# Kernel tuning notes

Measured on AMD Instinct MI355X. Metric: run time of the kernel, lower is better.

The kernel has to match this reference:

```python
import jax, jax.numpy as jnp
import numpy as np

P = 16
BN_EPS = 1e-5


def _to_patches(x, c, d):
    # [b, c*P, d*P] -> [b, c*d, P, P]
    b = x.shape[0]
    x = x.reshape(b, c, P, d, P).transpose(0, 1, 3, 2, 4)
    return x.reshape(b, c * d, P, P)


def _dwconv_block(x, dwk, g, bb, m, v, pwk):
    # depthwise 3x3 stride-2 conv (groups=C, no bias) + BN(eval) + GELU + 1x1 pointwise
    C = x.shape[1]
    y = jax.lax.conv_general_dilated(
        x, dwk[:, None, :, :], window_strides=(2, 2), padding=((1, 1), (1, 1)),
        feature_group_count=C, dimension_numbers=('NCHW', 'OIHW', 'NCHW'))
    y = g[None, :, None, None] * (y - m[None, :, None, None]) / jnp.sqrt(v + BN_EPS)[None, :, None, None] + bb[None, :, None, None]
    y = jax.nn.gelu(y, approximate=False)  # torch nn.GELU default = erf
    return jnp.einsum('bchw,oc->bohw', y, pwk)


def _forward(query, key, value, dw_k, bn_g, bn_b, bn_m, bn_v, pw_k, position, c1_w, c1_b, lin_w, lin_b):
    b, units, d_model = query.shape
    c = units // P
    d = d_model // P
    hp = P // 2  # spatial after stride-2 conv
    dk = hp * hp  # d_k = 64

    q = _to_patches(query, c, d)
    k = _to_patches(key, c, d)
    v = _to_patches(value, c, d)

    q = _dwconv_block(q, dw_k[0], bn_g[0], bn_b[0], bn_m[0], bn_v[0], pw_k[0])
    k = _dwconv_block(k, dw_k[1], bn_g[1], bn_b[1], bn_m[1], bn_v[1], pw_k[1])
    v = _dwconv_block(v, dw_k[2], bn_g[2], bn_b[2], bn_m[2], bn_v[2], pw_k[2])

    # [b, c*d, hp, hp] -> [b, c, d, hp*hp]
    q = q.reshape(b, c, d, dk)
    k = k.reshape(b, c, d, dk)
    v = v.reshape(b, c, d, dk)

    scores = jnp.einsum('bcdk,bcek->bcde', q, k) / jnp.sqrt(jnp.asarray(dk, q.dtype))
    scores = scores + position[None]  # learned additive position bias [c,d,d]
    p_attn = jax.nn.softmax(scores, axis=-1)
    x = jnp.einsum('bcde,bcek->bcdk', p_attn, v)  # [b, c, d, dk]

    # 'b c d (p1 p2) -> b (c p1) (d p2)', p1 = P//2
    x = x.reshape(b, c, d, hp, hp).transpose(0, 1, 3, 2, 4).reshape(b, c * hp, d * hp)

    # Conv1d(units//2 -> units, kernel 1) then Linear(d_model//2 -> d_model)
    x = jnp.einsum('bcl,oc->bol', x, c1_w) + c1_b[None, :, None]
    x = jnp.einsum('bcl,ol->bco', x, lin_w) + lin_b[None, None, :]
    return x


def setup_inputs() -> dict:
    key = jax.random.key(0)
    ks = jax.random.split(key, 8)
    b, units, d_model = 64, 32, 4096
    C = (units // P) * (d_model // P)  # 512
    inp = {
        'query': jax.random.normal(ks[0], (b, units, d_model), jnp.float32),
        'key': jax.random.normal(ks[1], (b, units, d_model), jnp.float32),
        'value': jax.random.normal(ks[2], (b, units, d_model), jnp.float32),
        'dw_k': jax.random.normal(ks[3], (3, C, 3, 3), jnp.float32) * 0.1,
        'bn_g': jnp.ones((3, C), jnp.float32),
        'bn_b': jnp.zeros((3, C), jnp.float32),
        'bn_m': jnp.zeros((3, C), jnp.float32),
        'bn_v': jnp.ones((3, C), jnp.float32),
        'pw_k': jax.random.normal(ks[4], (3, C, C), jnp.float32) * 0.02,
        'position': jax.random.normal(ks[5], (units // P, d_model // P, d_model // P), jnp.float32),
        'c1_w': jax.random.normal(ks[6], (units, units // 2), jnp.float32) * 0.1,
        'c1_b': jnp.zeros((units,), jnp.float32),
        'lin_w': jax.random.normal(ks[7], (d_model, d_model // 2), jnp.float32) * 0.02,
        'lin_b': jnp.zeros((d_model,), jnp.float32),
    }
    return inp


def reference(query, key, value, dw_k, bn_g, bn_b, bn_m, bn_v, pw_k, position, c1_w, c1_b, lin_w, lin_b):
    return _forward(query, key, value, dw_k, bn_g, bn_b, bn_m, bn_v, pw_k, position, c1_w, c1_b, lin_w, lin_b)
```

## Files before the change

### kernel.cpp

```cpp
#include <hip/hip_runtime.h>


typedef short s16x8 __attribute__((ext_vector_type(8)));
typedef float f32x4 __attribute__((ext_vector_type(4)));
typedef const __attribute__((address_space(1))) void* gas_t;
typedef __attribute__((address_space(3))) void* las_t;

__device__ __forceinline__ unsigned short f2bf(float x) {
  unsigned u = __float_as_uint(x);
  unsigned r = u + 0x7fffu + ((u >> 16) & 1u);
  return (unsigned short)(r >> 16);
}
__device__ __forceinline__ float bf2f(unsigned short h) {
  return __uint_as_float((unsigned)h << 16);
}

__global__ __launch_bounds__(256) void stageA_kernel(
    const float* __restrict__ xq, const float* __restrict__ xk,
    const float* __restrict__ xv, const float* __restrict__ dwk,
    const float* __restrict__ bng, const float* __restrict__ bnb,
    const float* __restrict__ bnm, const float* __restrict__ bnv,
    unsigned short* __restrict__ tTp)
{
  const int i  = blockIdx.y;
  const float* x = (i == 0) ? xq : (i == 1) ? xk : xv;
  const float* dwk_i = dwk + (size_t)i * 4608;
  const int co = i * 512;
  unsigned short* out = tTp + (size_t)i * 4194304;

  const int dd = threadIdx.x;
  const int oh = blockIdx.x & 7;
  const int cc = (blockIdx.x >> 3) & 1;
  const int b  = blockIdx.x >> 4;
  const int ch = cc * 256 + dd;

  float r[3][16];
#pragma unroll
  for (int kh = 0; kh < 3; ++kh) {
    int ih = 2 * oh - 1 + kh;
    if (ih >= 0 && ih <= 15) {
      const float* p = x + (size_t)(b * 32 + cc * 16 + ih) * 4096 + dd * 16;
#pragma unroll
      for (int jq = 0; jq < 4; ++jq)
        *(float4*)&r[kh][jq * 4] = *(const float4*)(p + jq * 4);
    } else {
#pragma unroll
      for (int j = 0; j < 16; ++j) r[kh][j] = 0.f;
    }
  }
  float w9[9];
#pragma unroll
  for (int j = 0; j < 9; ++j) w9[j] = dwk_i[ch * 9 + j];
  const float scale = bng[co + ch] / sqrtf(bnv[co + ch] + 1e-5f);
  const float shift = bnb[co + ch] - bnm[co + ch] * scale;

#pragma unroll
  for (int ow = 0; ow < 8; ++ow) {
    float acc = 0.f;
#pragma unroll
    for (int kh = 0; kh < 3; ++kh)
#pragma unroll
      for (int kw = 0; kw < 3; ++kw) {
        int iw = 2 * ow - 1 + kw;
        if (iw >= 0 && iw <= 15) acc = fmaf(r[kh][iw], w9[kh * 3 + kw], acc);
      }
    float y = acc * scale + shift;
    y = 0.5f * y * (1.f + erff(y * 0.70710678118654752f));
    unsigned short hi = f2bf(y);
    unsigned short lo = f2bf(y - bf2f(hi));
    size_t rowb = (size_t)(b * 64 + oh * 8 + ow) * 1024;
    out[rowb + ch] = hi;
    out[rowb + 512 + ch] = lo;
  }
}

__global__ __launch_bounds__(256) void split_kernel(
    const float* __restrict__ src, unsigned short* __restrict__ dst,
    int kshift, int total4)
{
  int i = blockIdx.x * 256 + threadIdx.x;
  if (i >= total4) return;
  size_t i4 = (size_t)i * 4;
  int K = 1 << kshift;
  int r = (int)(i4 >> kshift);
  int c = (int)(i4 & (size_t)(K - 1));
  float4 xv = *(const float4*)(src + i4);
  unsigned short h0 = f2bf(xv.x), h1 = f2bf(xv.y), h2 = f2bf(xv.z), h3 = f2bf(xv.w);
  unsigned short l0 = f2bf(xv.x - bf2f(h0)), l1 = f2bf(xv.y - bf2f(h1));
  unsigned short l2 = f2bf(xv.z - bf2f(h2)), l3 = f2bf(xv.w - bf2f(h3));
  unsigned short* dr = dst + (size_t)r * (K * 2) + c;
  uint2 hp, lp;
  hp.x = (unsigned)h0 | ((unsigned)h1 << 16);
  hp.y = (unsigned)h2 | ((unsigned)h3 << 16);
  lp.x = (unsigned)l0 | ((unsigned)l1 << 16);
  lp.y = (unsigned)l2 | ((unsigned)l3 << 16);
  *(uint2*)dr = hp;
  *(uint2*)(dr + K) = lp;
}

__global__ __launch_bounds__(256) void split_rs_kernel(
    const float* __restrict__ src, unsigned short* __restrict__ dst,
    float* __restrict__ rs, int total4)
{
  int i = blockIdx.x * 256 + threadIdx.x;
  if (i >= total4) return;
  size_t i4 = (size_t)i * 4;
  int r = (int)(i4 >> 11);
  int c = (int)(i4 & 2047);
  float4 xv = *(const float4*)(src + i4);
  unsigned short h0 = f2bf(xv.x), h1 = f2bf(xv.y), h2 = f2bf(xv.z), h3 = f2bf(xv.w);
  unsigned short l0 = f2bf(xv.x - bf2f(h0)), l1 = f2bf(xv.y - bf2f(h1));
  unsigned short l2 = f2bf(xv.z - bf2f(h2)), l3 = f2bf(xv.w - bf2f(h3));
  unsigned short* dr = dst + (size_t)r * 4096 + c;
  uint2 hp, lp;
  hp.x = (unsigned)h0 | ((unsigned)h1 << 16);
  hp.y = (unsigned)h2 | ((unsigned)h3 << 16);
  lp.x = (unsigned)l0 | ((unsigned)l1 << 16);
  lp.y = (unsigned)l2 | ((unsigned)l3 << 16);
  *(uint2*)dr = hp;
  *(uint2*)(dr + 2048) = lp;
  float s = xv.x + xv.y + xv.z + xv.w;
#pragma unroll
  for (int off = 1; off < 64; off <<= 1) s += __shfl_xor(s, off, 64);
  if ((threadIdx.x & 63) == 0) atomicAdd(&rs[r], s);
}

__global__ __launch_bounds__(256) void gemm_split_kernel(
    const unsigned short* __restrict__ Aall, const unsigned short* __restrict__ Ball,
    unsigned short* __restrict__ Call, int M, int N, int K)
{
  __shared__ unsigned short sA[4096];
  __shared__ unsigned short sB[8192];
  const int t = threadIdx.x;
  const int z = blockIdx.z;
  const unsigned short* A = Aall + (size_t)z * 524288;
  const unsigned short* B = Ball + (size_t)z * 4194304;
  unsigned short* Cq = Call + (size_t)z * 4194304;
  const int m0 = blockIdx.y * 64, n0 = blockIdx.x * 128;
  const int Kp = 3 * K, twoK = 2 * K, Km = K - 1;
  const int lane = t & 63;
  const int wv = t >> 6;
  const int colbase = wv * 32;
  const int h = lane & 15, g = lane >> 4;

  f32x4 acc[4][2];
#pragma unroll
  for (int mf = 0; mf < 4; ++mf)
#pragma unroll
    for (int nf = 0; nf < 2; ++nf)
      acc[mf][nf] = (f32x4){0.f, 0.f, 0.f, 0.f};

  int srow[4], sblk[4];
#pragma unroll
  for (int it = 0; it < 4; ++it) {
    int s = it * 256 + t;
    srow[it] = s >> 3;
    sblk[it] = (s & 7) ^ (srow[it] & 7);
  }
  const int ldsw = (t & 192) << 4;

  for (int k0 = 0; k0 < Kp; k0 += 64) {
    __syncthreads();
#pragma unroll
    for (int it = 0; it < 2; ++it) {
      int kp = k0 + sblk[it] * 8;
      int ac = (kp < twoK) ? (kp & Km) : (kp - K);
      const unsigned short* ga = A + (size_t)(m0 + srow[it]) * twoK + ac;
      __builtin_amdgcn_global_load_lds((gas_t)(const void*)ga,
          (las_t)(void*)((char*)sA + (it * 4096 + ldsw)), 16, 0, 0);
    }
#pragma unroll
    for (int it = 0; it < 4; ++it) {
      int kp = k0 + sblk[it] * 8;
      int bc = (kp < twoK) ? kp : (kp - twoK);
      const unsigned short* gb = B + (size_t)(n0 + srow[it]) * twoK + bc;
      __builtin_amdgcn_global_load_lds((gas_t)(const void*)gb,
          (las_t)(void*)((char*)sB + (it * 4096 + ldsw)), 16, 0, 0);
    }
    __syncthreads();

#pragma unroll
    for (int kk = 0; kk < 2; ++kk) {
      s16x8 af[4], bfr[2];
#pragma unroll
      for (int mf = 0; mf < 4; ++mf) {
        int arow = mf * 16 + h;
        int aoff = arow * 128 + (((kk * 4 + g) ^ (h & 7)) << 4);
        af[mf] = *(const s16x8*)((const char*)sA + aoff);
      }
#pragma unroll
      for (int nf = 0; nf < 2; ++nf) {
        int brow = colbase + nf * 16 + h;
        int boff = brow * 128 + (((kk * 4 + g) ^ (h & 7)) << 4);
        bfr[nf] = *(const s16x8*)((const char*)sB + boff);
      }
#pragma unroll
      for (int mf = 0; mf < 4; ++mf)
#pragma unroll
        for (int nf = 0; nf < 2; ++nf)
          acc[mf][nf] = __builtin_amdgcn_mfma_f32_16x16x32_bf16(
              af[mf], bfr[nf], acc[mf][nf], 0, 0, 0);
    }
  }

  if (z < 2) {
#pragma unroll
    for (int mf = 0; mf < 4; ++mf) {
      int mbase = m0 + mf * 16 + g * 4;
#pragma unroll
      for (int nf = 0; nf < 2; ++nf) {
        int n = n0 + colbase + nf * 16 + h;
        int bb = n >> 6, d = n & 63;
#pragma unroll
        for (int qq = 0; qq < 4; ++qq) {
          int m = mbase + qq;
          int cc = m >> 8;
          size_t rowb = ((size_t)(bb * 2 + cc) * 256 + (m & 255)) * 128;
          float vvv = acc[mf][nf][qq];
          unsigned short hi = f2bf(vvv);
          unsigned short lo = f2bf(vvv - bf2f(hi));
          Cq[rowb + d] = hi;
          Cq[rowb + 64 + d] = lo;
        }
      }
    }
  } else {
#pragma unroll
    for (int mf = 0; mf < 4; ++mf) {
      int mbase = m0 + mf * 16 + g * 4;
      int cc = mbase >> 8;
      int mc = mbase & 255;
#pragma unroll
      for (int nf = 0; nf < 2; ++nf) {
        int n = n0 + colbase + nf * 16 + h;
        int bb = n >> 6, d = n & 63;
        size_t rowb = ((size_t)(bb * 2 + cc) * 64 + d) * 512;
        ushort4 hv, lv;
        float v0 = acc[mf][nf][0], v1 = acc[mf][nf][1];
        float v2 = acc[mf][nf][2], v3 = acc[mf][nf][3];
        hv.x = f2bf(v0); hv.y = f2bf(v1); hv.z = f2bf(v2); hv.w = f2bf(v3);
        lv.x = f2bf(v0 - bf2f(hv.x)); lv.y = f2bf(v1 - bf2f(hv.y));
        lv.z = f2bf(v2 - bf2f(hv.z)); lv.w = f2bf(v3 - bf2f(hv.w));
        *(ushort4*)&Cq[rowb + mc] = hv;
        *(ushort4*)&Cq[rowb + 256 + mc] = lv;
      }
    }
  }
}

__global__ __launch_bounds__(512, 2) void gemm_final_kernel(
    const unsigned short* __restrict__ A, const unsigned short* __restrict__ B,
    float* __restrict__ C)
{
  __shared__ unsigned short lds[73728];
  const int t = threadIdx.x;

  const int flat = blockIdx.y * 32 + blockIdx.x;
  const int xcd = flat & 7;
  const int ii = flat >> 3;
  const int n0 = (xcd * 4 + (ii & 3)) * 128;
  const int rem = ii >> 2;
  const int m0 = (rem & 3) * 256;
  const int ks = rem >> 2;
  const int base = ks * 48;

  const int K = 2048, twoK = 4096, Km = 2047;

  const int lane = t & 63;
  const int wv = t >> 6;
  const int wm = wv & 3, wn = wv >> 2;
  const int h = lane & 15, g = lane >> 4;

  f32x4 acc[4][4];
#pragma unroll
  for (int mf = 0; mf < 4; ++mf)
#pragma unroll
    for (int nf = 0; nf < 4; ++nf)
      acc[mf][nf] = (f32x4){0.f, 0.f, 0.f, 0.f};

  int arow[4], ablk[4], brow[2], bblk[2];
#pragma unroll
  for (int it = 0; it < 4; ++it) {
    int s = it * 512 + t;
    arow[it] = s >> 3;
    ablk[it] = (t & 7) ^ (arow[it] & 7);
  }
#pragma unroll
  for (int it = 0; it < 2; ++it) {
    int s = it * 512 + t;
    brow[it] = s >> 3;
    bblk[it] = (t & 7) ^ (brow[it] & 7);
  }

  auto issueA = [&](int buf, int tt, int it) {
    int kp = tt * 64 + ablk[it] * 8;
    int ac = (kp < twoK) ? (kp & Km) : (kp - K);
    __builtin_amdgcn_global_load_lds(
        (gas_t)(const void*)(A + (size_t)(m0 + arow[it]) * twoK + ac),
        (las_t)(void*)((char*)lds + (buf * 49152 + it * 8192 + t * 16)), 16, 0, 0);
  };
  auto issueB = [&](int buf, int tt, int it) {
    int kp = tt * 64 + bblk[it] * 8;
    int bc = (kp < twoK) ? kp : (kp - twoK);
    __builtin_amdgcn_global_load_lds(
        (gas_t)(const void*)(B + (size_t)(n0 + brow[it]) * twoK + bc),
        (las_t)(void*)((char*)lds + (buf * 49152 + 32768 + it * 8192 + t * 16)), 16, 0, 0);
  };

  const int aoffb = (wm * 64 + h) * 128;
  const int boffb = 32768 + (wn * 64 + h) * 128;
  int colx[2];
  colx[0] = ((g) ^ (h & 7)) << 4;
  colx[1] = ((4 + g) ^ (h & 7)) << 4;

  auto rdA = [&](int buf, int kk, int mf) -> s16x8 {
    return *(const s16x8*)((const char*)lds + (buf * 49152 + aoffb + mf * 2048 + colx[kk]));
  };
  auto rdB = [&](int buf, int kk, int nf) -> s16x8 {
    return *(const s16x8*)((const char*)lds + (buf * 49152 + boffb + nf * 2048 + colx[kk]));
  };

#define MFMA_ROW2(A0, A1, A2, A3, BB, NF) \
  acc[0][NF] = __builtin_amdgcn_mfma_f32_16x16x32_bf16(A0, BB, acc[0][NF], 0, 0, 0); \
  acc[1][NF] = __builtin_amdgcn_mfma_f32_16x16x32_bf16(A1, BB, acc[1][NF], 0, 0, 0); \
  acc[2][NF] = __builtin_amdgcn_mfma_f32_16x16x32_bf16(A2, BB, acc[2][NF], 0, 0, 0); \
  acc[3][NF] = __builtin_amdgcn_mfma_f32_16x16x32_bf16(A3, BB, acc[3][NF], 0, 0, 0);

#pragma unroll
  for (int it = 0; it < 4; ++it) issueA(0, base, it);
#pragma unroll
  for (int it = 0; it < 2; ++it) issueB(0, base, it);
#pragma unroll
  for (int it = 0; it < 4; ++it) issueA(1, base + 1, it);
#pragma unroll
  for (int it = 0; it < 2; ++it) issueB(1, base + 1, it);
  asm volatile("s_waitcnt vmcnt(6)" ::: "memory");
  __builtin_amdgcn_sched_barrier(0);
  __builtin_amdgcn_s_barrier();
  __builtin_amdgcn_sched_barrier(0);

  int bR = 0;
  for (int tt = base; tt <= base + 45; ++tt) {
    const int bn2 = (bR >= 1) ? bR - 1 : 2;
    s16x8 a0 = rdA(bR, 0, 0), a1 = rdA(bR, 0, 1), a2 = rdA(bR, 0, 2), a3 = rdA(bR, 0, 3);
    s16x8 b0 = rdB(bR, 0, 0), b1 = rdB(bR, 0, 1);
    issueA(bn2, tt + 2, 0); issueA(bn2, tt + 2, 1);
    __builtin_amdgcn_s_barrier();
    __builtin_amdgcn_s_setprio(1);
    MFMA_ROW2(a0, a1, a2, a3, b0, 0)
    MFMA_ROW2(a0, a1, a2, a3, b1, 1)
    __builtin_amdgcn_s_setprio(0);
    __builtin_amdgcn_s_barrier();
    s16x8 b2 = rdB(bR, 0, 2), b3 = rdB(bR, 0, 3);
    issueA(bn2, tt + 2, 2); issueA(bn2, tt + 2, 3);
    __builtin_amdgcn_s_barrier();
    __builtin_amdgcn_s_setprio(1);
    MFMA_ROW2(a0, a1, a2, a3, b2, 2)
    MFMA_ROW2(a0, a1, a2, a3, b3, 3)
    __builtin_amdgcn_s_setprio(0);
    __builtin_amdgcn_s_barrier();
    a0 = rdA(bR, 1, 0); a1 = rdA(bR, 1, 1); a2 = rdA(bR, 1, 2); a3 = rdA(bR, 1, 3);
    b0 = rdB(bR, 1, 0); b1 = rdB(bR, 1, 1);
    issueB(bn2, tt + 2, 0);
    __builtin_amdgcn_s_barrier();
    __builtin_amdgcn_s_setprio(1);
    MFMA_ROW2(a0, a1, a2, a3, b0, 0)
    MFMA_ROW2(a0, a1, a2, a3, b1, 1)
    __builtin_amdgcn_s_setprio(0);
    __builtin_amdgcn_s_barrier();
    b2 = rdB(bR, 1, 2); b3 = rdB(bR, 1, 3);
    issueB(bn2, tt + 2, 1);
    __builtin_amdgcn_s_barrier();
    __builtin_amdgcn_s_setprio(1);
    MFMA_ROW2(a0, a1, a2, a3, b2, 2)
    MFMA_ROW2(a0, a1, a2, a3, b3, 3)
    __builtin_amdgcn_s_setprio(0);
    asm volatile("s_waitcnt vmcnt(6)" ::: "memory");
    __builtin_amdgcn_sched_barrier(0);
    __builtin_amdgcn_s_barrier();
    __builtin_amdgcn_sched_barrier(0);
    bR = (bR == 2) ? 0 : bR + 1;
  }

  auto compute_tile = [&](int buf) {
#pragma unroll
    for (int kk = 0; kk < 2; ++kk) {
      s16x8 ta0 = rdA(buf, kk, 0), ta1 = rdA(buf, kk, 1);
      s16x8 ta2 = rdA(buf, kk, 2), ta3 = rdA(buf, kk, 3);
      s16x8 tb0 = rdB(buf, kk, 0), tb1 = rdB(buf, kk, 1);
      s16x8 tb2 = rdB(buf, kk, 2), tb3 = rdB(buf, kk, 3);
      MFMA_ROW2(ta0, ta1, ta2, ta3, tb0, 0)
      MFMA_ROW2(ta0, ta1, ta2, ta3, tb1, 1)
      MFMA_ROW2(ta0, ta1, ta2, ta3, tb2, 2)
      MFMA_ROW2(ta0, ta1, ta2, ta3, tb3, 3)
    }
  };
  compute_tile(bR);
  __syncthreads();
  compute_tile((bR == 2) ? 0 : bR + 1);
#undef MFMA_ROW2

  float* Cks = C + (size_t)ks * 4194304;
#pragma unroll
  for (int mf = 0; mf < 4; ++mf) {
    int mbase = m0 + wm * 64 + mf * 16 + g * 4;
#pragma unroll
    for (int nf = 0; nf < 4; ++nf) {
      int n = n0 + wn * 64 + nf * 16 + h;
#pragma unroll
      for (int qq = 0; qq < 4; ++qq)
        Cks[(size_t)(mbase + qq) * 4096 + n] = acc[mf][nf][qq];
    }
  }
}

__global__ __launch_bounds__(256) void attn_mfma_kernel(
    const unsigned short* __restrict__ qp, const unsigned short* __restrict__ kp,
    const unsigned short* __restrict__ vtp, const float* __restrict__ pos,
    unsigned short* __restrict__ Xp)
{
  __shared__ char smem[59904];
  unsigned short* qs = (unsigned short*)smem;
  unsigned short* kv = (unsigned short*)(smem + 8704);
  float* sc = (float*)(smem + 26112);
  unsigned short* ps = (unsigned short*)(smem + 26112);

  const int t = threadIdx.x;
  const int rt = blockIdx.x, cc = blockIdx.y, b = blockIdx.z;
  const int i0 = rt * 32;
  const size_t qkbase = (size_t)(b * 2 + cc) * 256;
  const size_t vbase  = (size_t)(b * 2 + cc) * 64;

  const int lane = t & 63, wvv = t >> 6;
  const int h = lane & 15, g = lane >> 4;

#pragma unroll
  for (int rep = 0; rep < 2; ++rep) {
    int s = t + rep * 256;
    int row = s >> 4;
    int blk = s & 15;
    int4 val = *(const int4*)(qp + (qkbase + i0 + row) * 128 + blk * 8);
    *(int4*)((char*)qs + row * 272 + blk * 16) = val;
  }

  for (int c = 0; c < 4; ++c) {
    __syncthreads();
#pragma unroll
    for (int p2 = 0; p2 < 4; ++p2) {
      int s = t + p2 * 256;
      int row = s >> 4;
      int blk = s & 15;
      int4 val = *(const int4*)(kp + (qkbase + c * 64 + row) * 128 + blk * 8);
      *(int4*)((char*)kv + row * 272 + blk * 16) = val;
    }
    __syncthreads();
    f32x4 acc2[2];
    acc2[0] = (f32x4){0.f, 0.f, 0.f, 0.f};
    acc2[1] = (f32x4){0.f, 0.f, 0.f, 0.f};
#pragma unroll
    for (int kk = 0; kk < 6; ++kk) {
      int abase = (kk < 2) ? kk * 32 : (kk < 4) ? 64 + (kk - 2) * 32 : (kk - 4) * 32;
      int bbase = (kk < 2) ? kk * 32 : (kk < 4) ? (kk - 2) * 32 : 64 + (kk - 4) * 32;
      s16x8 bfrag = *(const s16x8*)((char*)kv + (wvv * 16 + h) * 272 + (bbase + g * 8) * 2);
#pragma unroll
      for (int mf = 0; mf < 2; ++mf) {
        s16x8 afrag = *(const s16x8*)((char*)qs + (mf * 16 + h) * 272 + (abase + g * 8) * 2);
        acc2[mf] = __builtin_amdgcn_mfma_f32_16x16x32_bf16(afrag, bfrag, acc2[mf], 0, 0, 0);
      }
    }
#pragma unroll
    for (int mf = 0; mf < 2; ++mf)
#pragma unroll
      for (int qq = 0; qq < 4; ++qq) {
        int row = mf * 16 + g * 4 + qq;
        int j = c * 64 + wvv * 16 + h;
        sc[row * 264 + j] = acc2[mf][qq] * 0.125f +
            pos[((size_t)cc * 256 + i0 + row) * 256 + j];
      }
  }
  __syncthreads();

  {
    const int r = t >> 3, j8 = t & 7;
    float e[32];
    float mx = -3.4e38f;
#pragma unroll
    for (int jj = 0; jj < 32; ++jj) {
      e[jj] = sc[r * 264 + j8 + 8 * jj];
      mx = fmaxf(mx, e[jj]);
    }
#pragma unroll
    for (int mset = 1; mset < 8; mset <<= 1) mx = fmaxf(mx, __shfl_xor(mx, mset, 64));
    float sum = 0.f;
#pragma unroll
    for (int jj = 0; jj < 32; ++jj) {
      e[jj] = expf(e[jj] - mx);
      sum += e[jj];
    }
#pragma unroll
    for (int mset = 1; mset < 8; mset <<= 1) sum += __shfl_xor(sum, mset, 64);
    float inv = 1.f / sum;
    __syncthreads();
#pragma unroll
    for (int jj = 0; jj < 32; ++jj) {
      float pv = e[jj] * inv;
      unsigned short hi = f2bf(pv);
      unsigned short lo = f2bf(pv - bf2f(hi));
      int j = j8 + 8 * jj;
      ps[r * 528 + j] = hi;
      ps[r * 528 + 264 + j] = lo;
    }
  }

  f32x4 oacc[2];
  oacc[0] = (f32x4){0.f, 0.f, 0.f, 0.f};
  oacc[1] = (f32x4){0.f, 0.f, 0.f, 0.f};
  for (int c = 0; c < 4; ++c) {
    __syncthreads();
#pragma unroll
    for (int p2 = 0; p2 < 4; ++p2) {
      int s = t + p2 * 256, row = s >> 4, blk = s & 15;
      int col = (blk < 8) ? (c * 64 + blk * 8) : (256 + c * 64 + (blk - 8) * 8);
      int4 val = *(const int4*)(vtp + (vbase + row) * 512 + col);
      *(int4*)((char*)kv + row * 272 + blk * 16) = val;
    }
    __syncthreads();
#pragma unroll
    for (int kk = 0; kk < 6; ++kk) {
      int abase = (kk < 2) ? (c * 64 + kk * 32)
                : (kk < 4) ? (264 + c * 64 + (kk - 2) * 32)
                           : (c * 64 + (kk - 4) * 32);
      int bbase = (kk < 2) ? kk * 32 : (kk < 4) ? (kk - 2) * 32 : 64 + (kk - 4) * 32;
      s16x8 bfrag = *(const s16x8*)((char*)kv + (wvv * 16 + h) * 272 + (bbase + g * 8) * 2);
#pragma unroll
      for (int mf = 0; mf < 2; ++mf) {
        s16x8 afrag = *(const s16x8*)((char*)ps + (mf * 16 + h) * 1056 + (abase + g * 8) * 2);
        oacc[mf] = __builtin_amdgcn_mfma_f32_16x16x32_bf16(afrag, bfrag, oacc[mf], 0, 0, 0);
      }
    }
  }
  {
    int Xrow = b * 16 + cc * 8 + wvv * 2 + (h >> 3);
    int c7 = h & 7;
#pragma unroll
    for (int mf = 0; mf < 2; ++mf)
#pragma unroll
      for (int qq = 0; qq < 4; ++qq) {
        int dd = i0 + mf * 16 + g * 4 + qq;
        float vvv = oacc[mf][qq];
        unsigned short hi = f2bf(vvv);
        unsigned short lo = f2bf(vvv - bf2f(hi));
        size_t base = (size_t)Xrow * 4096 + dd * 8 + c7;
        Xp[base] = hi;
        Xp[base + 2048] = lo;
      }
  }
}

__global__ __launch_bounds__(256) void epilogue_kernel(
    const float* __restrict__ G, const float* __restrict__ rs,
    const float* __restrict__ c1w, const float* __restrict__ c1b,
    const float* __restrict__ linb, float* __restrict__ out)
{
  __shared__ float W[512];
  __shared__ float Bp[32];
  const int t = threadIdx.x;
  const int ntile = blockIdx.x;
  const int b = blockIdx.y;
  W[t] = c1w[t];
  W[t + 256] = c1w[t + 256];
  if (t < 32) Bp[t] = c1b[t];
  __syncthreads();
  const int n = ntile * 256 + t;
  float gv[16];
#pragma unroll
  for (int ch = 0; ch < 16; ++ch) {
    size_t off = (size_t)(b * 16 + ch) * 4096 + n;
    gv[ch] = G[off] + G[4194304 + off];
  }
  const float rsn = rs[n];
  const float lbn = linb[n];
#pragma unroll
  for (int o = 0; o < 32; ++o) {
    float s = lbn + Bp[o] * rsn;
#pragma unroll
    for (int ch = 0; ch < 16; ++ch) s = fmaf(W[o * 16 + ch], gv[ch], s);
    out[(size_t)(b * 32 + o) * 4096 + n] = s;
  }
}

extern "C" void kernel_launch(void* const* d_in, const int* in_sizes, int n_in,
                              void* d_out, int out_size, void* d_ws, size_t ws_size,
                              hipStream_t stream) {
  const float* q    = (const float*)d_in[0];
  const float* k    = (const float*)d_in[1];
  const float* v    = (const float*)d_in[2];
  const float* dwk  = (const float*)d_in[3];
  const float* bng  = (const float*)d_in[4];
  const float* bnb  = (const float*)d_in[5];
  const float* bnm  = (const float*)d_in[6];
  const float* bnv  = (const float*)d_in[7];
  const float* pwk  = (const float*)d_in[8];
  const float* pos  = (const float*)d_in[9];
  const float* c1w  = (const float*)d_in[10];
  const float* c1b  = (const float*)d_in[11];
  const float* linw = (const float*)d_in[12];
  const float* linb = (const float*)d_in[13];
  float* out = (float*)d_out;

  if (ws_size < 50331648u) return;

  char* ws = (char*)d_ws;
  unsigned short* qp   = (unsigned short*)(ws + 0);
  unsigned short* kpp  = (unsigned short*)(ws + 8388608);
  unsigned short* vtp  = (unsigned short*)(ws + 16777216);
  unsigned short* tTp  = (unsigned short*)(ws + 25165824);
  unsigned short* pwkp = (unsigned short*)d_out;
  unsigned short* Xp   = (unsigned short*)(ws + 41943040);
  float*          rs   = (float*)(ws + 0);
  unsigned short* lwp  = (unsigned short*)d_out;
  float*          G    = (float*)(ws + 8388608);

  split_kernel<<<768, 256, 0, stream>>>(pwk, pwkp, 9, 196608);

  stageA_kernel<<<dim3(1024, 3), 256, 0, stream>>>(
      q, k, v, dwk, bng, bnb, bnm, bnv, tTp);

  gemm_split_kernel<<<dim3(32, 8, 3), 256, 0, stream>>>(
      pwkp, tTp, qp, 512, 4096, 512);

  attn_mfma_kernel<<<dim3(8, 2, 64), 256, 0, stream>>>(qp, kpp, vtp, pos, Xp);

  hipMemsetAsync(rs, 0, 16384, stream);
  split_rs_kernel<<<8192, 256, 0, stream>>>(linw, lwp, rs, 2097152);

  gemm_final_kernel<<<dim3(32, 8), 512, 0, stream>>>(Xp, lwp, G);

  epilogue_kernel<<<dim3(16, 64), 256, 0, stream>>>(G, rs, c1w, c1b, linb, out);
}
```

Before: 182.6 us.

## Give each split-GEMM wave a wider tile and compute row sums per block without atomics

The split GEMM now runs 2 waves per block instead of 4, and each wave computes a 64x64 output tile (4x4 MFMA fragments) rather than 64x32. This raises fragment reuse from LDS per wave but halves the waves per block. The row-sum split kernel now gives one block to each weight row, writes 8 elements per thread, and reduces through shared memory. That removes both the memset and the global atomics. Shapes are hardcoded as constants.

```diff
diff --git a/kernel.cpp b/kernel.cpp
--- a/kernel.cpp
+++ b/kernel.cpp
@@ -100,34 +100,39 @@
 
 __global__ __launch_bounds__(256) void split_rs_kernel(
     const float* __restrict__ src, unsigned short* __restrict__ dst,
-    float* __restrict__ rs, int total4)
+    float* __restrict__ rs)
 {
-  int i = blockIdx.x * 256 + threadIdx.x;
-  if (i >= total4) return;
-  size_t i4 = (size_t)i * 4;
-  int r = (int)(i4 >> 11);
-  int c = (int)(i4 & 2047);
-  float4 xv = *(const float4*)(src + i4);
-  unsigned short h0 = f2bf(xv.x), h1 = f2bf(xv.y), h2 = f2bf(xv.z), h3 = f2bf(xv.w);
-  unsigned short l0 = f2bf(xv.x - bf2f(h0)), l1 = f2bf(xv.y - bf2f(h1));
-  unsigned short l2 = f2bf(xv.z - bf2f(h2)), l3 = f2bf(xv.w - bf2f(h3));
-  unsigned short* dr = dst + (size_t)r * 4096 + c;
-  uint2 hp, lp;
+  __shared__ float wsum[4];
+  const int r = blockIdx.x;
+  const int t = threadIdx.x;
+  const float* rowp = src + (size_t)r * 2048 + t * 8;
+  float4 x0 = *(const float4*)rowp;
+  float4 x1 = *(const float4*)(rowp + 4);
+  unsigned short h0 = f2bf(x0.x), h1 = f2bf(x0.y), h2 = f2bf(x0.z), h3 = f2bf(x0.w);
+  unsigned short h4 = f2bf(x1.x), h5 = f2bf(x1.y), h6 = f2bf(x1.z), h7 = f2bf(x1.w);
+  uint4 hp, lp;
   hp.x = (unsigned)h0 | ((unsigned)h1 << 16);
   hp.y = (unsigned)h2 | ((unsigned)h3 << 16);
-  lp.x = (unsigned)l0 | ((unsigned)l1 << 16);
-  lp.y = (unsigned)l2 | ((unsigned)l3 << 16);
-  *(uint2*)dr = hp;
-  *(uint2*)(dr + 2048) = lp;
-  float s = xv.x + xv.y + xv.z + xv.w;
+  hp.z = (unsigned)h4 | ((unsigned)h5 << 16);
+  hp.w = (unsigned)h6 | ((unsigned)h7 << 16);
+  lp.x = (unsigned)f2bf(x0.x - bf2f(h0)) | ((unsigned)f2bf(x0.y - bf2f(h1)) << 16);
+  lp.y = (unsigned)f2bf(x0.z - bf2f(h2)) | ((unsigned)f2bf(x0.w - bf2f(h3)) << 16);
+  lp.z = (unsigned)f2bf(x1.x - bf2f(h4)) | ((unsigned)f2bf(x1.y - bf2f(h5)) << 16);
+  lp.w = (unsigned)f2bf(x1.z - bf2f(h6)) | ((unsigned)f2bf(x1.w - bf2f(h7)) << 16);
+  unsigned short* dr = dst + (size_t)r * 4096 + t * 8;
+  *(uint4*)dr = hp;
+  *(uint4*)(dr + 2048) = lp;
+  float s = x0.x + x0.y + x0.z + x0.w + x1.x + x1.y + x1.z + x1.w;
 #pragma unroll
   for (int off = 1; off < 64; off <<= 1) s += __shfl_xor(s, off, 64);
-  if ((threadIdx.x & 63) == 0) atomicAdd(&rs[r], s);
-}
-
-__global__ __launch_bounds__(256) void gemm_split_kernel(
+  if ((t & 63) == 0) wsum[t >> 6] = s;
+  __syncthreads();
+  if (t == 0) rs[r] = wsum[0] + wsum[1] + wsum[2] + wsum[3];
+}
+
+__global__ __launch_bounds__(128) void gemm_split_kernel(
     const unsigned short* __restrict__ Aall, const unsigned short* __restrict__ Ball,
-    unsigned short* __restrict__ Call, int M, int N, int K)
+    unsigned short* __restrict__ Call)
 {
   __shared__ unsigned short sA[4096];
   __shared__ unsigned short sB[8192];
@@ -137,67 +142,70 @@
   const unsigned short* B = Ball + (size_t)z * 4194304;
   unsigned short* Cq = Call + (size_t)z * 4194304;
   const int m0 = blockIdx.y * 64, n0 = blockIdx.x * 128;
-  const int Kp = 3 * K, twoK = 2 * K, Km = K - 1;
+  const int K = 512, twoK = 1024, Km = 511;
   const int lane = t & 63;
   const int wv = t >> 6;
-  const int colbase = wv * 32;
+  const int colbase = wv * 64;
   const int h = lane & 15, g = lane >> 4;
 
-  f32x4 acc[4][2];
+  f32x4 acc[4][4];
 #pragma unroll
   for (int mf = 0; mf < 4; ++mf)
 #pragma unroll
-    for (int nf = 0; nf < 2; ++nf)
+    for (int nf = 0; nf < 4; ++nf)
       acc[mf][nf] = (f32x4){0.f, 0.f, 0.f, 0.f};
 
-  int srow[4], sblk[4];
+  int arow[4], ablk[4], brow[8], bblk[8];
 #pragma unroll
   for (int it = 0; it < 4; ++it) {
-    int s = it * 256 + t;
-    srow[it] = s >> 3;
-    sblk[it] = (s & 7) ^ (srow[it] & 7);
-  }
-  const int ldsw = (t & 192) << 4;
-
-  for (int k0 = 0; k0 < Kp; k0 += 64) {
+    int s = it * 128 + t;
+    arow[it] = s >> 3;
+    ablk[it] = (s & 7) ^ (arow[it] & 7);
+  }
+#pragma unroll
+  for (int it = 0; it < 8; ++it) {
+    int s = it * 128 + t;
+    brow[it] = s >> 3;
+    bblk[it] = (s & 7) ^ (brow[it] & 7);
+  }
+
+  for (int k0 = 0; k0 < 1536; k0 += 64) {
     __syncthreads();
 #pragma unroll
-    for (int it = 0; it < 2; ++it) {
-      int kp = k0 + sblk[it] * 8;
+    for (int it = 0; it < 4; ++it) {
+      int kp = k0 + ablk[it] * 8;
       int ac = (kp < twoK) ? (kp & Km) : (kp - K);
-      const unsigned short* ga = A + (size_t)(m0 + srow[it]) * twoK + ac;
-      __builtin_amdgcn_global_load_lds((gas_t)(const void*)ga,
-          (las_t)(void*)((char*)sA + (it * 4096 + ldsw)), 16, 0, 0);
-    }
-#pragma unroll
-    for (int it = 0; it < 4; ++it) {
-      int kp = k0 + sblk[it] * 8;
+      __builtin_amdgcn_global_load_lds(
+          (gas_t)(const void*)(A + (size_t)(m0 + arow[it]) * twoK + ac),
+          (las_t)(void*)((char*)sA + (it * 2048 + t * 16)), 16, 0, 0);
+    }
+#pragma unroll
+    for (int it = 0; it < 8; ++it) {
+      int kp = k0 + bblk[it] * 8;
       int bc = (kp < twoK) ? kp : (kp - twoK);
-      const unsigned short* gb = B + (size_t)(n0 + srow[it]) * twoK + bc;
-      __builtin_amdgcn_global_load_lds((gas_t)(const void*)gb,
-          (las_t)(void*)((char*)sB + (it * 4096 + ldsw)), 16, 0, 0);
+      __builtin_amdgcn_global_load_lds(
+          (gas_t)(const void*)(B + (size_t)(n0 + brow[it]) * twoK + bc),
+          (las_t)(void*)((char*)sB + (it * 2048 + t * 16)), 16, 0, 0);
     }
     __syncthreads();
 
 #pragma unroll
     for (int kk = 0; kk < 2; ++kk) {
-      s16x8 af[4], bfr[2];
+      s16x8 af[4], bfr[4];
 #pragma unroll
       for (int mf = 0; mf < 4; ++mf) {
-        int arow = mf * 16 + h;
-        int aoff = arow * 128 + (((kk * 4 + g) ^ (h & 7)) << 4);
+        int aoff = (mf * 16 + h) * 128 + (((kk * 4 + g) ^ (h & 7)) << 4);
         af[mf] = *(const s16x8*)((const char*)sA + aoff);
       }
 #pragma unroll
-      for (int nf = 0; nf < 2; ++nf) {
-        int brow = colbase + nf * 16 + h;
-        int boff = brow * 128 + (((kk * 4 + g) ^ (h & 7)) << 4);
+      for (int nf = 0; nf < 4; ++nf) {
+        int boff = (colbase + nf * 16 + h) * 128 + (((kk * 4 + g) ^ (h & 7)) << 4);
         bfr[nf] = *(const s16x8*)((const char*)sB + boff);
       }
 #pragma unroll
       for (int mf = 0; mf < 4; ++mf)
 #pragma unroll
-        for (int nf = 0; nf < 2; ++nf)
+        for (int nf = 0; nf < 4; ++nf)
           acc[mf][nf] = __builtin_amdgcn_mfma_f32_16x16x32_bf16(
               af[mf], bfr[nf], acc[mf][nf], 0, 0, 0);
     }
@@ -208,7 +216,7 @@
     for (int mf = 0; mf < 4; ++mf) {
       int mbase = m0 + mf * 16 + g * 4;
 #pragma unroll
-      for (int nf = 0; nf < 2; ++nf) {
+      for (int nf = 0; nf < 4; ++nf) {
         int n = n0 + colbase + nf * 16 + h;
         int bb = n >> 6, d = n & 63;
 #pragma unroll
@@ -231,7 +239,7 @@
       int cc = mbase >> 8;
       int mc = mbase & 255;
 #pragma unroll
-      for (int nf = 0; nf < 2; ++nf) {
+      for (int nf = 0; nf < 4; ++nf) {
         int n = n0 + colbase + nf * 16 + h;
         int bb = n >> 6, d = n & 63;
         size_t rowb = ((size_t)(bb * 2 + cc) * 64 + d) * 512;
@@ -626,13 +634,11 @@
   stageA_kernel<<<dim3(1024, 3), 256, 0, stream>>>(
       q, k, v, dwk, bng, bnb, bnm, bnv, tTp);
 
-  gemm_split_kernel<<<dim3(32, 8, 3), 256, 0, stream>>>(
-      pwkp, tTp, qp, 512, 4096, 512);
+  gemm_split_kernel<<<dim3(32, 8, 3), 128, 0, stream>>>(pwkp, tTp, qp);
 
   attn_mfma_kernel<<<dim3(8, 2, 64), 256, 0, stream>>>(qp, kpp, vtp, pos, Xp);
 
-  hipMemsetAsync(rs, 0, 16384, stream);
-  split_rs_kernel<<<8192, 256, 0, stream>>>(linw, lwp, rs, 2097152);
+  split_rs_kernel<<<4096, 256, 0, stream>>>(linw, lwp, rs);
 
   gemm_final_kernel<<<dim3(32, 8), 512, 0, stream>>>(Xp, lwp, G);
 
```

After: 180.5 us. About the same (-1.2%).
